# Optimization experiments

Hardware: AMD Instinct MI355X
Metric: run time of the kernel (lower is better)

The kernel has to match this reference:

```python
import jax, jax.numpy as jnp
import numpy as np

N, E, R, L = 50000, 800000, 2, 4
IN, HID, H, D, OUT = 64, 128, 8, 16, 32
EPS = 1e-5


def setup_inputs() -> dict:
    key = jax.random.key(0)
    ks = jax.random.split(key, 12)
    inp = {
        "inputs": jax.random.normal(ks[0], (N, IN), jnp.float32),
        "src": jax.random.randint(ks[1], (R, E), 0, N, jnp.int32),
        "dst": jax.random.randint(ks[2], (R, E), 0, N, jnp.int32),
        "embed_w1": jax.random.normal(ks[3], (IN, HID), jnp.float32) / np.sqrt(IN),
        "embed_gamma": jnp.ones((HID,), jnp.float32),
        "embed_beta": jnp.zeros((HID,), jnp.float32),
        "embed_w2": jax.random.normal(ks[4], (HID, HID), jnp.float32) / np.sqrt(HID),
        "gat_fc": jax.random.normal(ks[5], (L, R, HID, HID), jnp.float32) / np.sqrt(HID),
        "gat_attn_l": jax.random.normal(ks[6], (L, R, H, D), jnp.float32) * 0.1,
        "gat_attn_r": jax.random.normal(ks[7], (L, R, H, D), jnp.float32) * 0.1,
        "gat_bias": jnp.zeros((L, R, HID), jnp.float32),
        "dec_w1": jax.random.normal(ks[8], (HID, HID), jnp.float32) / np.sqrt(HID),
        "dec_gamma": jnp.ones((HID,), jnp.float32),
        "dec_beta": jnp.zeros((HID,), jnp.float32),
        "dec_w2": jax.random.normal(ks[9], (HID, OUT), jnp.float32) / np.sqrt(HID),
    }
    return inp


def _bn(x, gamma, beta):
    # BatchNorm1d in training mode: batch statistics, biased variance
    mean = jnp.mean(x, axis=0)
    var = jnp.mean(jnp.square(x - mean), axis=0)
    return (x - mean) * jax.lax.rsqrt(var + EPS) * gamma + beta


def _gat(h, s, d, W, al, ar, b):
    # DGL GATConv: fc -> per-head attention logits -> edge softmax over dst -> scatter-sum
    feat = (h @ W).reshape(N, H, D)                      # [N,H,D]
    el = jnp.sum(feat * al, axis=-1)                     # [N,H]
    er = jnp.sum(feat * ar, axis=-1)                     # [N,H]
    e = jax.nn.leaky_relu(el[s] + er[d], 0.2)            # [E,H]
    emax = jax.ops.segment_max(e, d, num_segments=N)     # [N,H]
    ex = jnp.exp(e - emax[d])
    denom = jax.ops.segment_sum(ex, d, num_segments=N)   # [N,H]
    alpha = ex / denom[d]                                # [E,H]
    msg = feat[s] * alpha[:, :, None]                    # [E,H,D]
    rst = jax.ops.segment_sum(msg, d, num_segments=N)    # [N,H,D]
    return rst + b.reshape(H, D)


def reference(inputs, src, dst, embed_w1, embed_gamma, embed_beta, embed_w2,
              gat_fc, gat_attn_l, gat_attn_r, gat_bias,
              dec_w1, dec_gamma, dec_beta, dec_w2):
    # MLP2 embed: relu(bn(x@w1)); out = h@w2 + h (residual)
    h = jax.nn.relu(_bn(inputs @ embed_w1, embed_gamma, embed_beta))
    h1 = h @ embed_w2 + h                                # [N,HID]
    for l in range(L):
        acc = jnp.zeros((N, H, D), h1.dtype)
        for r in range(R):  # HeteroGraphConv aggregate='sum'
            acc = acc + _gat(h1, src[r], dst[r], gat_fc[l, r],
                             gat_attn_l[l, r], gat_attn_r[l, r], gat_bias[l, r])
        h2 = jax.nn.leaky_relu(acc, 0.01).reshape(N, HID)
        h1 = h2 + h1                                     # residual
    # decision MLP: relu(bn(h@w1)) @ w2
    hd = jax.nn.relu(_bn(h1 @ dec_w1, dec_gamma, dec_beta))
    return hd @ dec_w2                                   # [N,OUT]
```

## Files before the change

### kernel.cpp

```cpp
#include <hip/hip_runtime.h>
#include <hip/hip_fp16.h>
#include <math.h>

#define NN 50000
#define EE 800000
#define NHEAD 8
#define BN_EPS 1e-5f
#define NBIN 196
#define NBLK 64
#define EPB (EE / NBLK)
#define SCT (2 * NBIN * NBLK)
#define SCHUNK 98

typedef _Float16 half8_t __attribute__((ext_vector_type(8)));
typedef float float4_t __attribute__((ext_vector_type(4)));

__device__ __forceinline__ unsigned fenc(float f) {
  unsigned u = __float_as_uint(f);
  return (u & 0x80000000u) ? ~u : (u | 0x80000000u);
}
__device__ __forceinline__ float fdec(unsigned k) {
  return (k & 0x80000000u) ? __uint_as_float(k & 0x7fffffffu)
                           : __uint_as_float(~k);
}

__device__ __forceinline__ void bn_coef(const float* __restrict__ stats,
                                        const float* __restrict__ gamma,
                                        const float* __restrict__ beta,
                                        int c, float& sc, float& sh) {
  float mean = stats[c] * (1.f / NN);
  float var = fmaxf(stats[128 + c] * (1.f / NN) - mean * mean, 0.f);
  sc = gamma[c] * rsqrtf(var + BN_EPS);
  sh = beta[c] - mean * sc;
}

template <int PAT>
__device__ __forceinline__ float ds_swz(float x) {
  return __int_as_float(__builtin_amdgcn_ds_swizzle(__float_as_int(x), PAT));
}

template <int KDIM, int NC, typename AT, bool ABN, bool RESIDBN, bool STATS,
          bool F16OUT, bool F32OUT>
__global__ __launch_bounds__(256)
void mfma_gemm_k(const AT* __restrict__ A, const _Float16* __restrict__ Bt,
                 const float* __restrict__ bn, const float* __restrict__ gamma,
                 const float* __restrict__ beta, float* __restrict__ statsOut,
                 const _Float16* __restrict__ residh, _Float16* __restrict__ Ch,
                 float* __restrict__ Cf, int M) {
  constexpr int NT = NC / 16;
  const int lane = threadIdx.x & 63, wave = threadIdx.x >> 6;
  const int q = lane >> 4, l16 = lane & 15;
  const int row0 = blockIdx.x * 128 + wave * 32;
  float4_t acc[2][NT];
#pragma unroll
  for (int i = 0; i < 2; ++i)
#pragma unroll
    for (int j = 0; j < NT; ++j) acc[i][j] = (float4_t){0.f, 0.f, 0.f, 0.f};

#pragma unroll
  for (int kk = 0; kk < KDIM / 32; ++kk) {
    float scv[8], shv[8];
    if constexpr (ABN) {
      int kb = kk * 32 + q * 8;
#pragma unroll
      for (int x = 0; x < 8; ++x) bn_coef(bn, gamma, beta, kb + x, scv[x], shv[x]);
    }
    half8_t a[2];
#pragma unroll
    for (int i = 0; i < 2; ++i) {
      int r = row0 + i * 16 + l16;
      r = (r < M) ? r : (M - 1);
      if constexpr (__is_same(AT, _Float16)) {
        half8_t hv = *(const half8_t*)(A + (size_t)r * KDIM + kk * 32 + q * 8);
        if constexpr (ABN) {
#pragma unroll
          for (int x = 0; x < 8; ++x)
            hv[x] = (_Float16)fmaxf((float)hv[x] * scv[x] + shv[x], 0.f);
        }
        a[i] = hv;
      } else {
        const float* ap = (const float*)A + (size_t)r * KDIM + kk * 32 + q * 8;
        float4 v0 = *(const float4*)ap, v1 = *(const float4*)(ap + 4);
        float t[8] = {v0.x, v0.y, v0.z, v0.w, v1.x, v1.y, v1.z, v1.w};
        if constexpr (ABN) {
#pragma unroll
          for (int x = 0; x < 8; ++x) t[x] = fmaxf(t[x] * scv[x] + shv[x], 0.f);
        }
        half8_t hv;
#pragma unroll
        for (int x = 0; x < 8; ++x) hv[x] = (_Float16)t[x];
        a[i] = hv;
      }
    }
#pragma unroll
    for (int j = 0; j < NT; ++j) {
      half8_t b = *(const half8_t*)(Bt + (size_t)(j * 16 + l16) * KDIM + kk * 32 + q * 8);
      acc[0][j] = __builtin_amdgcn_mfma_f32_16x16x32_f16(a[0], b, acc[0][j], 0, 0, 0);
      acc[1][j] = __builtin_amdgcn_mfma_f32_16x16x32_f16(a[1], b, acc[1][j], 0, 0, 0);
    }
  }

  float rsc[NT], rsh[NT];
  if constexpr (RESIDBN) {
#pragma unroll
    for (int j = 0; j < NT; ++j) bn_coef(bn, gamma, beta, j * 16 + l16, rsc[j], rsh[j]);
  }
#pragma unroll
  for (int i = 0; i < 2; ++i)
#pragma unroll
    for (int r = 0; r < 4; ++r) {
      int row = row0 + i * 16 + q * 4 + r;
      if (row >= M) continue;
      float vv[NT];
#pragma unroll
      for (int j = 0; j < NT; ++j) {
        float v = acc[i][j][r];
        if constexpr (RESIDBN) {
          float rv = (float)residh[(size_t)row * NC + j * 16 + l16];
          v += fmaxf(rv * rsc[j] + rsh[j], 0.f);
        }
        vv[j] = v;
        if constexpr (F32OUT) Cf[(size_t)row * NC + j * 16 + l16] = v;
      }
      if constexpr (F16OUT) {
        const bool ev = (l16 & 1) == 0;
#pragma unroll
        for (int jp = 0; jp < NT / 2; ++jp) {
          float a_ = vv[2 * jp], b_ = vv[2 * jp + 1];
          float an = ds_swz<(1 << 10) | 0x1F>(a_);
          float bn_ = ds_swz<(1 << 10) | 0x1F>(b_);
          float lo = ev ? a_ : bn_;
          float hi = ev ? an : b_;
          int jj = ev ? 2 * jp : 2 * jp + 1;
          __half2 hv = __floats2half2_rn(lo, hi);
          ((__half2*)Ch)[((size_t)row * NC + jj * 16 + (l16 & ~1)) >> 1] = hv;
        }
      }
    }

  if constexpr (STATS) {
    static_assert(!STATS || NT == 8, "stats layout assumes NC=128");
    __shared__ float reds[256];
    reds[threadIdx.x] = 0.f;
    __syncthreads();
    float sc_[NT], sq_[NT];
#pragma unroll
    for (int j = 0; j < NT; ++j) {
      float s = 0.f, qq = 0.f;
#pragma unroll
      for (int i = 0; i < 2; ++i)
#pragma unroll
        for (int r = 0; r < 4; ++r) {
          int row = row0 + i * 16 + q * 4 + r;
          float x = (row < M) ? acc[i][j][r] : 0.f;
          s += x; qq += x * x;
        }
      sc_[j] = s; sq_[j] = qq;
    }
#pragma unroll
    for (int j = 0; j < NT; ++j) {
      sc_[j] += __shfl_xor(sc_[j], 16, 64);
      sq_[j] += __shfl_xor(sq_[j], 16, 64);
      sc_[j] += __shfl_xor(sc_[j], 32, 64);
      sq_[j] += __shfl_xor(sq_[j], 32, 64);
    }
    if (lane < 16) {
#pragma unroll
      for (int j = 0; j < NT; ++j) {
        atomicAdd(&reds[j * 16 + l16], sc_[j]);
        atomicAdd(&reds[128 + j * 16 + l16], sq_[j]);
      }
    }
    __syncthreads();
    atomicAdd(&statsOut[threadIdx.x], reds[threadIdx.x]);
  }
}

__global__ __launch_bounds__(256)
void feat_gemm_k(const _Float16* __restrict__ A, const _Float16* __restrict__ Bt,
                 _Float16* __restrict__ feat0, _Float16* __restrict__ feat1,
                 _Float16* __restrict__ el0h, float* __restrict__ er0,
                 _Float16* __restrict__ el1h, float* __restrict__ er1,
                 unsigned* __restrict__ elmax, int M) {
  constexpr int NT = 18;
  const int lane = threadIdx.x & 63, wave = threadIdx.x >> 6;
  const int q = lane >> 4, l16 = lane & 15;
  const int row0 = blockIdx.x * 128 + wave * 32;
  __shared__ unsigned redm[16];
  if (threadIdx.x < 16) redm[threadIdx.x] = 0u;
  float4_t acc[2][NT];
#pragma unroll
  for (int i = 0; i < 2; ++i)
#pragma unroll
    for (int j = 0; j < NT; ++j) acc[i][j] = (float4_t){0.f, 0.f, 0.f, 0.f};

#pragma unroll
  for (int kk = 0; kk < 4; ++kk) {
    half8_t a[2];
#pragma unroll
    for (int i = 0; i < 2; ++i) {
      int r = row0 + i * 16 + l16;
      r = (r < M) ? r : (M - 1);
      a[i] = *(const half8_t*)(A + (size_t)r * 128 + kk * 32 + q * 8);
    }
#pragma unroll
    for (int j = 0; j < NT; ++j) {
      half8_t b = *(const half8_t*)(Bt + (size_t)(j * 16 + l16) * 128 + kk * 32 + q * 8);
      acc[0][j] = __builtin_amdgcn_mfma_f32_16x16x32_f16(a[0], b, acc[0][j], 0, 0, 0);
      acc[1][j] = __builtin_amdgcn_mfma_f32_16x16x32_f16(a[1], b, acc[1][j], 0, 0, 0);
    }
  }

#pragma unroll
  for (int i = 0; i < 2; ++i)
#pragma unroll
    for (int r = 0; r < 4; ++r) {
      int row = row0 + i * 16 + q * 4 + r;
      if (row >= M) continue;
      const bool ev = (l16 & 1) == 0;
#pragma unroll
      for (int jp = 0; jp < 8; ++jp) {
        float a_ = acc[i][2 * jp][r], b_ = acc[i][2 * jp + 1][r];
        float an = ds_swz<(1 << 10) | 0x1F>(a_);
        float bn_ = ds_swz<(1 << 10) | 0x1F>(b_);
        float lo = ev ? a_ : bn_;
        float hi = ev ? an : b_;
        int jj = ev ? 2 * jp : 2 * jp + 1;
        __half2 hv = __floats2half2_rn(lo, hi);
        _Float16* fb = (jj < 8) ? feat0 : feat1;
        int colbase = (jj < 8) ? jj * 16 : (jj - 8) * 16;
        ((__half2*)fb)[((size_t)row * 128 + colbase + (l16 & ~1)) >> 1] = hv;
      }
      {
        float v = acc[i][16][r];
        if (l16 < 8) el0h[(size_t)row * 8 + l16] = (_Float16)v;
        else         er0[(size_t)row * 8 + (l16 - 8)] = v;
        v = acc[i][17][r];
        if (l16 < 8) el1h[(size_t)row * 8 + l16] = (_Float16)v;
        else         er1[(size_t)row * 8 + (l16 - 8)] = v;
      }
    }

  float m0 = -1e30f, m1 = -1e30f;
#pragma unroll
  for (int i = 0; i < 2; ++i)
#pragma unroll
    for (int r = 0; r < 4; ++r) {
      m0 = fmaxf(m0, acc[i][16][r]);
      m1 = fmaxf(m1, acc[i][17][r]);
    }
  m0 = fmaxf(m0, __shfl_xor(m0, 16, 64)); m0 = fmaxf(m0, __shfl_xor(m0, 32, 64));
  m1 = fmaxf(m1, __shfl_xor(m1, 16, 64)); m1 = fmaxf(m1, __shfl_xor(m1, 32, 64));
  __syncthreads();
  if (q == 0 && l16 < 8) {
    atomicMax(&redm[l16], fenc(m0));
    atomicMax(&redm[8 + l16], fenc(m1));
  }
  __syncthreads();
  if (threadIdx.x < 16) atomicMax(&elmax[threadIdx.x], redm[threadIdx.x]);
}

__global__ __launch_bounds__(256)
void build_k(const float* __restrict__ ew1, const float* __restrict__ ew2,
             const float* __restrict__ dw1, const float* __restrict__ dw2,
             const float* __restrict__ gfc, const float* __restrict__ gal,
             const float* __restrict__ gar, _Float16* __restrict__ ew1t,
             _Float16* __restrict__ ew2t, _Float16* __restrict__ dw1t,
             _Float16* __restrict__ dw2t, _Float16* __restrict__ bt,
             float* __restrict__ statsz, unsigned* __restrict__ elmax,
             const int* __restrict__ dstIdx, int* __restrict__ bcnt) {
  const int bid = blockIdx.x;

  if (bid < 172) {
    const float* src; _Float16* dst; int K, N, kt, ct;
    if (bid < 8)       { src = ew1; dst = ew1t; K = 64;  N = 128; int t = bid;      kt = t >> 2; ct = t & 3; }
    else if (bid < 24) { src = ew2; dst = ew2t; K = 128; N = 128; int t = bid - 8;  kt = t >> 2; ct = t & 3; }
    else if (bid < 40) { src = dw1; dst = dw1t; K = 128; N = 128; int t = bid - 24; kt = t >> 2; ct = t & 3; }
    else if (bid < 44) { src = dw2; dst = dw2t; K = 128; N = 32;  int t = bid - 40; kt = t;      ct = 0;     }
    else {
      int idx = bid - 44;
      int mat = idx >> 4, t = idx & 15;
      int b = mat >> 1, r = mat & 1;
      src = gfc + (size_t)(2 * b + r) * 16384;
      dst = bt + (size_t)b * 288 * 128 + (size_t)r * 128 * 128;
      K = 128; N = 128; kt = t >> 2; ct = t & 3;
    }
    __shared__ float tile[32][33];
    int k0 = kt * 32, c0 = ct * 32;
    int tk = threadIdx.x >> 5, tc = threadIdx.x & 31;
#pragma unroll
    for (int it = 0; it < 4; ++it) {
      int k = k0 + tk + it * 8;
      tile[tc][tk + it * 8] = src[(size_t)k * N + c0 + tc];
    }
    __syncthreads();
    int ci = threadIdx.x >> 5, ck = threadIdx.x & 31;
#pragma unroll
    for (int it = 0; it < 4; ++it) {
      int c = c0 + ci + it * 8;
      dst[(size_t)c * K + k0 + ck] = (_Float16)tile[ci + it * 8][ck];
    }
  } else if (bid < 176) {
    int b = bid - 172;
    _Float16* dstL = bt + (size_t)b * 288 * 128;
    for (int idx = threadIdx.x; idx < 32 * 128; idx += 256) {
      int c = 256 + (idx >> 7), k = idx & 127;
      int sub = c - 256, blk = sub >> 3, h = sub & 7;
      int r = blk >> 1;
      const float* attn = (blk & 1) ? gar : gal;
      const float* W = gfc + (size_t)(2 * b + r) * 16384;
      const float* av = attn + (size_t)(2 * b + r) * 128 + h * 16;
      float s = 0.f;
#pragma unroll
      for (int d = 0; d < 16; ++d) s += W[k * 128 + h * 16 + d] * av[d];
      dstL[c * 128 + k] = (_Float16)s;
    }
  } else if (bid == 176) {
    if (threadIdx.x < 64) elmax[threadIdx.x] = 0u;
    for (int i = threadIdx.x; i < 1024; i += 256) statsz[i] = 0.f;
  } else {
    int j = bid - 177;
    int r = j >> 6, blk = j & 63;
    __shared__ int bins[NBIN];
    for (int i = threadIdx.x; i < NBIN; i += 256) bins[i] = 0;
    __syncthreads();
    const int* d = dstIdx + (size_t)r * EE;
    int e0 = blk * EPB;
    for (int e = e0 + threadIdx.x; e < e0 + EPB; e += 256)
      atomicAdd(&bins[d[e] >> 8], 1);
    __syncthreads();
    for (int i = threadIdx.x; i < NBIN; i += 256)
      bcnt[(size_t)(r * NBIN + i) * NBLK + blk] = bins[i];
  }
}

__global__ __launch_bounds__(256)
void scanA_k(int* __restrict__ bcnt, int* __restrict__ totals) {
  __shared__ int sh[256];
  int b = blockIdx.x, t = threadIdx.x;
  int idx = b * 256 + t;
  int v = bcnt[idx];
  sh[t] = v;
  __syncthreads();
#pragma unroll
  for (int off = 1; off < 256; off <<= 1) {
    int tv = (t >= off) ? sh[t - off] : 0;
    __syncthreads();
    sh[t] += tv;
    __syncthreads();
  }
  bcnt[idx] = sh[t] - v;
  if (t == 255) totals[b] = sh[t];
}

__global__ __launch_bounds__(128)
void scanB_k(const int* __restrict__ totals, int* __restrict__ boff) {
  __shared__ int sh[128];
  int t = threadIdx.x;
  int v = (t < SCHUNK) ? totals[t] : 0;
  sh[t] = v;
  __syncthreads();
#pragma unroll
  for (int off = 1; off < 128; off <<= 1) {
    int tv = (t >= off) ? sh[t - off] : 0;
    __syncthreads();
    sh[t] += tv;
    __syncthreads();
  }
  if (t < SCHUNK) boff[t] = sh[t] - v;
}

__global__ __launch_bounds__(256)
void bscat_k(const int* __restrict__ src, const int* __restrict__ dst,
             const int* __restrict__ bcnt, const int* __restrict__ boff,
             unsigned* __restrict__ packed) {
  int r = blockIdx.y, blk = blockIdx.x;
  __shared__ int base[NBIN];
  for (int i = threadIdx.x; i < NBIN; i += 256) {
    int idx = (r * NBIN + i) * NBLK + blk;
    base[i] = bcnt[idx] + boff[idx >> 8];
  }
  __syncthreads();
  const int* d = dst + (size_t)r * EE;
  const int* s = src + (size_t)r * EE;
  int e0 = blk * EPB;
  for (int e = e0 + threadIdx.x; e < e0 + EPB; e += 256) {
    int dd = d[e];
    int pos = atomicAdd(&base[dd >> 8], 1);
    packed[pos] = (unsigned)s[e] | ((unsigned)dd << 16);
  }
}

__global__ __launch_bounds__(256)
void bfin_k(const unsigned* __restrict__ packed, const int* __restrict__ bcnt,
            const int* __restrict__ boff, int* __restrict__ rowptr,
            unsigned short* __restrict__ csr) {
  int f = blockIdx.x;
  int r = f / NBIN, b = f % NBIN;
  __shared__ int deg[256], pref[256], pos[256];
  int start = bcnt[(size_t)f * NBLK] + boff[(f * NBLK) >> 8];
  int end = (f + 1 < 2 * NBIN)
                ? (bcnt[(size_t)(f + 1) * NBLK] + boff[((f + 1) * NBLK) >> 8])
                : 2 * EE;
  deg[threadIdx.x] = 0;
  __syncthreads();
  for (int e = start + threadIdx.x; e < end; e += 256)
    atomicAdd(&deg[(packed[e] >> 16) & 255], 1);
  __syncthreads();
  int v = deg[threadIdx.x];
  pref[threadIdx.x] = v;
  __syncthreads();
#pragma unroll
  for (int off = 1; off < 256; off <<= 1) {
    int tv = (threadIdx.x >= off) ? pref[threadIdx.x - off] : 0;
    __syncthreads();
    pref[threadIdx.x] += tv;
    __syncthreads();
  }
  int excl = pref[threadIdx.x] - v;
  int node = b * 256 + threadIdx.x;
  if (node < NN) rowptr[r * (NN + 1) + node] = start - r * EE + excl;
  if (node == NN) rowptr[r * (NN + 1) + NN] = EE;
  pos[threadIdx.x] = start + excl;
  __syncthreads();
  for (int e = start + threadIdx.x; e < end; e += 256) {
    unsigned pk = packed[e];
    int local = (pk >> 16) & 255;
    int p = atomicAdd(&pos[local], 1);
    csr[p] = (unsigned short)(pk & 0xffffu);
  }
}

__global__ __launch_bounds__(256)
void gat_agg_k(const __half2* __restrict__ f0, const __half2* __restrict__ f1,
               const _Float16* __restrict__ el0h, const float* __restrict__ er0,
               const _Float16* __restrict__ el1h, const float* __restrict__ er1,
               const int* __restrict__ rowptr, const unsigned short* __restrict__ csr,
               const float* __restrict__ b0, const float* __restrict__ b1,
               const unsigned* __restrict__ elmax,
               _Float16* __restrict__ h1h) {
  int n = blockIdx.x * 4 + (threadIdx.x >> 6);
  if (n >= NN) return;
  int lane = threadIdx.x & 63;
  int head = lane >> 3, eslot = lane & 7;
  float er0h = er0[(size_t)n * 8 + head];
  float er1h = er1[(size_t)n * 8 + head];
  float bnd0 = fdec(elmax[head]) + er0h;       bnd0 = fmaxf(bnd0, 0.2f * bnd0);
  float bnd1 = fdec(elmax[8 + head]) + er1h;   bnd1 = fmaxf(bnd1, 0.2f * bnd1);
  int beg0 = rowptr[n], end0 = rowptr[n + 1];
  const int* rp1 = rowptr + (NN + 1);
  int beg1 = rp1[n], end1 = rp1[n + 1];
  const unsigned short* csr1 = csr + EE;
  int len = max(end0 - beg0, end1 - beg1);

  float ls0 = 0.f, a00 = 0.f, a01 = 0.f;
  float ls1 = 0.f, a10 = 0.f, a11 = 0.f;
  for (int t = 0; t < len; t += 8) {
    int t0 = beg0 + t, t1 = beg1 + t;
    int so0 = (int)csr[max(min(t0 + eslot, end0 - 1), 0)];
    int so1 = (int)csr1[max(min(t1 + eslot, end1 - 1), 0)];
    float ev0 = (float)el0h[(size_t)so0 * 8 + head];
    float ev1 = (float)el1h[(size_t)so1 * 8 + head];

    __half2 g0[8], g1[8];
#define LDJ(J)                                                          \
    {                                                                   \
      int sj0 = __builtin_amdgcn_ds_swizzle(so0, ((J) << 5) | 0x18);    \
      int sj1 = __builtin_amdgcn_ds_swizzle(so1, ((J) << 5) | 0x18);    \
      g0[J] = f0[(size_t)sj0 * 64 + lane];                              \
      g1[J] = f1[(size_t)sj1 * 64 + lane];                              \
    }
    LDJ(0) LDJ(1) LDJ(2) LDJ(3) LDJ(4) LDJ(5) LDJ(6) LDJ(7)
#undef LDJ

    float e0 = ev0 + er0h; e0 = fmaxf(e0, 0.2f * e0);
    float p0 = __expf(e0 - bnd0);
    p0 = (t0 + eslot < end0) ? p0 : 0.f;
    float e1 = ev1 + er1h; e1 = fmaxf(e1, 0.2f * e1);
    float p1 = __expf(e1 - bnd1);
    p1 = (t1 + eslot < end1) ? p1 : 0.f;
    ls0 += p0; ls1 += p1;

#define ACCJ(J)                                                     \
    {                                                               \
      float pj0 = ds_swz<((J) << 5) | 0x18>(p0);                    \
      float pj1 = ds_swz<((J) << 5) | 0x18>(p1);                    \
      a00 = fmaf(__low2float(g0[J]), pj0, a00);                     \
      a01 = fmaf(__high2float(g0[J]), pj0, a01);                    \
      a10 = fmaf(__low2float(g1[J]), pj1, a10);                     \
      a11 = fmaf(__high2float(g1[J]), pj1, a11);                    \
    }
    ACCJ(0) ACCJ(1) ACCJ(2) ACCJ(3) ACCJ(4) ACCJ(5) ACCJ(6) ACCJ(7)
#undef ACCJ
  }

  ls0 += ds_swz<(1 << 10) | 0x1F>(ls0);
  ls0 += ds_swz<(2 << 10) | 0x1F>(ls0);
  ls0 += ds_swz<(4 << 10) | 0x1F>(ls0);
  ls1 += ds_swz<(1 << 10) | 0x1F>(ls1);
  ls1 += ds_swz<(2 << 10) | 0x1F>(ls1);
  ls1 += ds_swz<(4 << 10) | 0x1F>(ls1);

  float inv0 = (ls0 > 0.f) ? 1.f / ls0 : 0.f;
  float inv1 = (ls1 > 0.f) ? 1.f / ls1 : 0.f;
  float t0 = a00 * inv0 + a10 * inv1 + b0[lane * 2] + b1[lane * 2];
  float t1 = a01 * inv0 + a11 * inv1 + b0[lane * 2 + 1] + b1[lane * 2 + 1];
  t0 = (t0 > 0.f) ? t0 : 0.01f * t0;
  t1 = (t1 > 0.f) ? t1 : 0.01f * t1;
  __half2* hh = (__half2*)h1h + (size_t)n * 64 + lane;
  float2 h = __half22float2(*hh);
  h.x += t0; h.y += t1;
  *hh = __floats2half2_rn(h.x, h.y);
}

extern "C" void kernel_launch(void* const* d_in, const int* in_sizes, int n_in,
                              void* d_out, int out_size, void* d_ws,
                              size_t ws_size, hipStream_t stream) {
  const float* inputs = (const float*)d_in[0];
  const int* src = (const int*)d_in[1];
  const int* dst = (const int*)d_in[2];
  const float* ew1 = (const float*)d_in[3];
  const float* eg = (const float*)d_in[4];
  const float* eb = (const float*)d_in[5];
  const float* ew2 = (const float*)d_in[6];
  const float* gfc = (const float*)d_in[7];
  const float* gal = (const float*)d_in[8];
  const float* gar = (const float*)d_in[9];
  const float* gb = (const float*)d_in[10];
  const float* dw1 = (const float*)d_in[11];
  const float* dg = (const float*)d_in[12];
  const float* db = (const float*)d_in[13];
  const float* dw2 = (const float*)d_in[14];
  float* out = (float*)d_out;

  char* p = (char*)d_ws;
  _Float16* feat0h = (_Float16*)p;
  _Float16* feat1h = feat0h + (size_t)NN * 128;
  _Float16* ybuf_h = feat0h;
  p += (size_t)NN * 128 * 4;
  _Float16* h1h = (_Float16*)p;     p += (size_t)NN * 128 * 2;
  _Float16* el0h = (_Float16*)p;    p += (size_t)NN * NHEAD * 2;
  float* er0 = (float*)p;           p += (size_t)NN * NHEAD * 4;
  _Float16* el1h = (_Float16*)p;    p += (size_t)NN * NHEAD * 2;
  float* er1 = (float*)p;           p += (size_t)NN * NHEAD * 4;
  float* stats = (float*)p;         p += 1024 * 4;
  float* stats_e = stats;
  float* stats_d = stats + 512;
  _Float16* ew1t = (_Float16*)p;    p += (size_t)64 * 128 * 2;
  _Float16* ew2t = (_Float16*)p;    p += (size_t)128 * 128 * 2;
  _Float16* dw1t = (_Float16*)p;    p += (size_t)128 * 128 * 2;
  _Float16* dw2t = (_Float16*)p;    p += (size_t)32 * 128 * 2;
  _Float16* bt = (_Float16*)p;      p += (size_t)4 * 288 * 128 * 2;
  int* rowptr = (int*)p;            p += (size_t)2 * (NN + 1) * 4;
  unsigned short* csr = (unsigned short*)p;   p += (size_t)2 * EE * 2;
  unsigned* packed = (unsigned*)p;  p += (size_t)2 * EE * 4;
  int* bcnt = (int*)p;              p += (size_t)SCT * 4;
  int* totals = (int*)p;            p += 128 * 4;
  int* boff = (int*)p;              p += 128 * 4;
  unsigned* elmaxAll = (unsigned*)p;

  const int GB = (NN + 127) / 128;

  build_k<<<305, 256, 0, stream>>>(ew1, ew2, dw1, dw2, gfc, gal, gar,
                                   ew1t, ew2t, dw1t, dw2t, bt, stats, elmaxAll,
                                   dst, bcnt);
  scanA_k<<<SCHUNK, 256, 0, stream>>>(bcnt, totals);
  scanB_k<<<1, 128, 0, stream>>>(totals, boff);
  bscat_k<<<dim3(NBLK, 2), 256, 0, stream>>>(src, dst, bcnt, boff, packed);
  bfin_k<<<2 * NBIN, 256, 0, stream>>>(packed, bcnt, boff, rowptr, csr);

  mfma_gemm_k<64, 128, float, false, false, true, true, false>
      <<<GB, 256, 0, stream>>>(inputs, ew1t, nullptr, nullptr, nullptr,
                               stats_e, nullptr, ybuf_h, nullptr, NN);
  mfma_gemm_k<128, 128, _Float16, true, true, false, true, false>
      <<<GB, 256, 0, stream>>>(ybuf_h, ew2t, stats_e, eg, eb, nullptr,
                               ybuf_h, h1h, nullptr, NN);

  for (int l = 0; l < 4; ++l) {
    unsigned* elm = elmaxAll + l * 16;
    feat_gemm_k<<<GB, 256, 0, stream>>>(
        h1h, bt + (size_t)l * 288 * 128, feat0h, feat1h,
        el0h, er0, el1h, er1, elm, NN);
    gat_agg_k<<<(NN + 3) / 4, 256, 0, stream>>>(
        (const __half2*)feat0h, (const __half2*)feat1h, el0h, er0, el1h, er1,
        rowptr, csr, gb + (size_t)(l * 2 + 0) * 128,
        gb + (size_t)(l * 2 + 1) * 128, elm, h1h);
  }

  mfma_gemm_k<128, 128, _Float16, false, false, true, true, false>
      <<<GB, 256, 0, stream>>>(h1h, dw1t, nullptr, nullptr, nullptr, stats_d,
                               nullptr, ybuf_h, nullptr, NN);
  mfma_gemm_k<128, 32, _Float16, true, false, false, false, true>
      <<<GB, 256, 0, stream>>>(ybuf_h, dw2t, stats_d, dg, db, nullptr,
                               nullptr, nullptr, out, NN);
}
```

Measured before the change: 625.7 us.

## Fold chunk-offset scan into consumers and software-pipeline GAT index loads

Removes the single-block scanB kernel launch: each block of bscat_k and bfin_k now recomputes the 98 chunk prefix offsets in shared memory from totals. In gat_agg_k, the CSR source indices are prefetched two iterations ahead and the el attention logits one iteration ahead, so the dependent index->logit->feature gather chain is overlapped across loop iterations. This trades a kernel launch and its serialization for redundant per-block scans, and adds register pressure plus some out-of-range-clamped extra loads in the aggregation loop.

```diff
diff --git a/kernel.cpp b/kernel.cpp
--- a/kernel.cpp
+++ b/kernel.cpp
@@ -353,32 +353,35 @@
   if (t == 255) totals[b] = sh[t];
 }
 
-__global__ __launch_bounds__(128)
-void scanB_k(const int* __restrict__ totals, int* __restrict__ boff) {
-  __shared__ int sh[128];
+__device__ __forceinline__ void chunk_offsets(const int* __restrict__ totals,
+                                              int* __restrict__ boffs) {
+  __shared__ int sh[256];
   int t = threadIdx.x;
   int v = (t < SCHUNK) ? totals[t] : 0;
   sh[t] = v;
   __syncthreads();
 #pragma unroll
-  for (int off = 1; off < 128; off <<= 1) {
+  for (int off = 1; off < 256; off <<= 1) {
     int tv = (t >= off) ? sh[t - off] : 0;
     __syncthreads();
     sh[t] += tv;
     __syncthreads();
   }
-  if (t < SCHUNK) boff[t] = sh[t] - v;
+  if (t < SCHUNK) boffs[t] = sh[t] - v;
+  __syncthreads();
 }
 
 __global__ __launch_bounds__(256)
 void bscat_k(const int* __restrict__ src, const int* __restrict__ dst,
-             const int* __restrict__ bcnt, const int* __restrict__ boff,
+             const int* __restrict__ bcnt, const int* __restrict__ totals,
              unsigned* __restrict__ packed) {
   int r = blockIdx.y, blk = blockIdx.x;
   __shared__ int base[NBIN];
+  __shared__ int boffs[SCHUNK];
+  chunk_offsets(totals, boffs);
   for (int i = threadIdx.x; i < NBIN; i += 256) {
     int idx = (r * NBIN + i) * NBLK + blk;
-    base[i] = bcnt[idx] + boff[idx >> 8];
+    base[i] = bcnt[idx] + boffs[idx >> 8];
   }
   __syncthreads();
   const int* d = dst + (size_t)r * EE;
@@ -393,14 +396,16 @@
 
 __global__ __launch_bounds__(256)
 void bfin_k(const unsigned* __restrict__ packed, const int* __restrict__ bcnt,
-            const int* __restrict__ boff, int* __restrict__ rowptr,
+            const int* __restrict__ totals, int* __restrict__ rowptr,
             unsigned short* __restrict__ csr) {
   int f = blockIdx.x;
   int r = f / NBIN, b = f % NBIN;
+  __shared__ int boffs[SCHUNK];
+  chunk_offsets(totals, boffs);
   __shared__ int deg[256], pref[256], pos[256];
-  int start = bcnt[(size_t)f * NBLK] + boff[(f * NBLK) >> 8];
+  int start = bcnt[(size_t)f * NBLK] + boffs[(f * NBLK) >> 8];
   int end = (f + 1 < 2 * NBIN)
-                ? (bcnt[(size_t)(f + 1) * NBLK] + boff[((f + 1) * NBLK) >> 8])
+                ? (bcnt[(size_t)(f + 1) * NBLK] + boffs[((f + 1) * NBLK) >> 8])
                 : 2 * EE;
   deg[threadIdx.x] = 0;
   __syncthreads();
@@ -453,32 +458,41 @@
   const unsigned short* csr1 = csr + EE;
   int len = max(end0 - beg0, end1 - beg1);
 
+#define CLAMP0(X) max(min((X), end0 - 1), 0)
+#define CLAMP1(X) max(min((X), end1 - 1), 0)
+  int sA0 = (int)csr[CLAMP0(beg0 + eslot)];
+  int sA1 = (int)csr1[CLAMP1(beg1 + eslot)];
+  int sB0 = (int)csr[CLAMP0(beg0 + 8 + eslot)];
+  int sB1 = (int)csr1[CLAMP1(beg1 + 8 + eslot)];
+  float evA0 = (float)el0h[(size_t)sA0 * 8 + head];
+  float evA1 = (float)el1h[(size_t)sA1 * 8 + head];
+
   float ls0 = 0.f, a00 = 0.f, a01 = 0.f;
   float ls1 = 0.f, a10 = 0.f, a11 = 0.f;
   for (int t = 0; t < len; t += 8) {
-    int t0 = beg0 + t, t1 = beg1 + t;
-    int so0 = (int)csr[max(min(t0 + eslot, end0 - 1), 0)];
-    int so1 = (int)csr1[max(min(t1 + eslot, end1 - 1), 0)];
-    float ev0 = (float)el0h[(size_t)so0 * 8 + head];
-    float ev1 = (float)el1h[(size_t)so1 * 8 + head];
+    int sC0 = (int)csr[CLAMP0(beg0 + t + 16 + eslot)];
+    int sC1 = (int)csr1[CLAMP1(beg1 + t + 16 + eslot)];
+    float evB0 = (float)el0h[(size_t)sB0 * 8 + head];
+    float evB1 = (float)el1h[(size_t)sB1 * 8 + head];
 
     __half2 g0[8], g1[8];
 #define LDJ(J)                                                          \
     {                                                                   \
-      int sj0 = __builtin_amdgcn_ds_swizzle(so0, ((J) << 5) | 0x18);    \
-      int sj1 = __builtin_amdgcn_ds_swizzle(so1, ((J) << 5) | 0x18);    \
+      int sj0 = __builtin_amdgcn_ds_swizzle(sA0, ((J) << 5) | 0x18);    \
+      int sj1 = __builtin_amdgcn_ds_swizzle(sA1, ((J) << 5) | 0x18);    \
       g0[J] = f0[(size_t)sj0 * 64 + lane];                              \
       g1[J] = f1[(size_t)sj1 * 64 + lane];                              \
     }
     LDJ(0) LDJ(1) LDJ(2) LDJ(3) LDJ(4) LDJ(5) LDJ(6) LDJ(7)
 #undef LDJ
 
-    float e0 = ev0 + er0h; e0 = fmaxf(e0, 0.2f * e0);
+    int i0 = beg0 + t + eslot, i1 = beg1 + t + eslot;
+    float e0 = evA0 + er0h; e0 = fmaxf(e0, 0.2f * e0);
     float p0 = __expf(e0 - bnd0);
-    p0 = (t0 + eslot < end0) ? p0 : 0.f;
-    float e1 = ev1 + er1h; e1 = fmaxf(e1, 0.2f * e1);
+    p0 = (i0 < end0) ? p0 : 0.f;
+    float e1 = evA1 + er1h; e1 = fmaxf(e1, 0.2f * e1);
     float p1 = __expf(e1 - bnd1);
-    p1 = (t1 + eslot < end1) ? p1 : 0.f;
+    p1 = (i1 < end1) ? p1 : 0.f;
     ls0 += p0; ls1 += p1;
 
 #define ACCJ(J)                                                     \
@@ -492,7 +506,12 @@
     }
     ACCJ(0) ACCJ(1) ACCJ(2) ACCJ(3) ACCJ(4) ACCJ(5) ACCJ(6) ACCJ(7)
 #undef ACCJ
-  }
+
+    sA0 = sB0; sA1 = sB1; sB0 = sC0; sB1 = sC1;
+    evA0 = evB0; evA1 = evB1;
+  }
+#undef CLAMP0
+#undef CLAMP1
 
   ls0 += ds_swz<(1 << 10) | 0x1F>(ls0);
   ls0 += ds_swz<(2 << 10) | 0x1F>(ls0);
@@ -556,7 +575,6 @@
   unsigned* packed = (unsigned*)p;  p += (size_t)2 * EE * 4;
   int* bcnt = (int*)p;              p += (size_t)SCT * 4;
   int* totals = (int*)p;            p += 128 * 4;
-  int* boff = (int*)p;              p += 128 * 4;
   unsigned* elmaxAll = (unsigned*)p;
 
   const int GB = (NN + 127) / 128;
@@ -565,9 +583,8 @@
                                    ew1t, ew2t, dw1t, dw2t, bt, stats, elmaxAll,
                                    dst, bcnt);
   scanA_k<<<SCHUNK, 256, 0, stream>>>(bcnt, totals);
-  scanB_k<<<1, 128, 0, stream>>>(totals, boff);
-  bscat_k<<<dim3(NBLK, 2), 256, 0, stream>>>(src, dst, bcnt, boff, packed);
-  bfin_k<<<2 * NBIN, 256, 0, stream>>>(packed, bcnt, boff, rowptr, csr);
+  bscat_k<<<dim3(NBLK, 2), 256, 0, stream>>>(src, dst, bcnt, totals, packed);
+  bfin_k<<<2 * NBIN, 256, 0, stream>>>(packed, bcnt, totals, rowptr, csr);
 
   mfma_gemm_k<64, 128, float, false, false, true, true, false>
       <<<GB, 256, 0, stream>>>(inputs, ew1t, nullptr, nullptr, nullptr,
```

Measured after the change: 631.4 us. No clear change (+0.9%).

## Fold embed GEMM into setup kernel and inline chunk-offset scan

Applied to the files above, without the earlier changes.

The first embedding GEMM (inputs @ ew1 with BatchNorm statistics) now runs as extra blocks of the setup kernel, which builds ew1 in fp16 directly in shared memory. The separate scanB kernel is removed, and each bscat/bfin block recomputes the chunk offsets from the totals itself. Stats zeroing moves to a memset. Together these cut two kernel launches and let the embed GEMM overlap the histogram work, at the cost of redundant per-block scans and a larger, more register- and LDS-heavy setup kernel.

```diff
diff --git a/kernel.cpp b/kernel.cpp
--- a/kernel.cpp
+++ b/kernel.cpp
@@ -260,6 +260,108 @@
   if (threadIdx.x < 16) atomicMax(&elmax[threadIdx.x], redm[threadIdx.x]);
 }
 
+__device__ __forceinline__ void embed1_block(
+    const float* __restrict__ A, const float* __restrict__ ew1,
+    float* __restrict__ statsOut, _Float16* __restrict__ Ch, int gb, int M) {
+  constexpr int NT = 8, BS = 72;
+  __shared__ _Float16 blds[128 * BS];
+  __shared__ float reds[256];
+  for (int L = threadIdx.x; L < 128 * 64; L += 256) {
+    int c = L >> 6, k = L & 63;
+    blds[c * BS + k] = (_Float16)ew1[k * 128 + c];
+  }
+  reds[threadIdx.x] = 0.f;
+  __syncthreads();
+
+  const int lane = threadIdx.x & 63, wave = threadIdx.x >> 6;
+  const int q = lane >> 4, l16 = lane & 15;
+  const int row0 = gb * 128 + wave * 32;
+  float4_t acc[2][NT];
+#pragma unroll
+  for (int i = 0; i < 2; ++i)
+#pragma unroll
+    for (int j = 0; j < NT; ++j) acc[i][j] = (float4_t){0.f, 0.f, 0.f, 0.f};
+
+#pragma unroll
+  for (int kk = 0; kk < 2; ++kk) {
+    half8_t a[2];
+#pragma unroll
+    for (int i = 0; i < 2; ++i) {
+      int r = row0 + i * 16 + l16;
+      r = (r < M) ? r : (M - 1);
+      const float* ap = A + (size_t)r * 64 + kk * 32 + q * 8;
+      float4 v0 = *(const float4*)ap, v1 = *(const float4*)(ap + 4);
+      float t[8] = {v0.x, v0.y, v0.z, v0.w, v1.x, v1.y, v1.z, v1.w};
+      half8_t hv;
+#pragma unroll
+      for (int x = 0; x < 8; ++x) hv[x] = (_Float16)t[x];
+      a[i] = hv;
+    }
+#pragma unroll
+    for (int j = 0; j < NT; ++j) {
+      half8_t b = *(const half8_t*)(blds + (size_t)(j * 16 + l16) * BS + kk * 32 + q * 8);
+      acc[0][j] = __builtin_amdgcn_mfma_f32_16x16x32_f16(a[0], b, acc[0][j], 0, 0, 0);
+      acc[1][j] = __builtin_amdgcn_mfma_f32_16x16x32_f16(a[1], b, acc[1][j], 0, 0, 0);
+    }
+  }
+
+#pragma unroll
+  for (int i = 0; i < 2; ++i)
+#pragma unroll
+    for (int r = 0; r < 4; ++r) {
+      int row = row0 + i * 16 + q * 4 + r;
+      if (row >= M) continue;
+      float vv[NT];
+#pragma unroll
+      for (int j = 0; j < NT; ++j) vv[j] = acc[i][j][r];
+      const bool ev = (l16 & 1) == 0;
+#pragma unroll
+      for (int jp = 0; jp < NT / 2; ++jp) {
+        float a_ = vv[2 * jp], b_ = vv[2 * jp + 1];
+        float an = ds_swz<(1 << 10) | 0x1F>(a_);
+        float bn_ = ds_swz<(1 << 10) | 0x1F>(b_);
+        float lo = ev ? a_ : bn_;
+        float hi = ev ? an : b_;
+        int jj = ev ? 2 * jp : 2 * jp + 1;
+        __half2 hv = __floats2half2_rn(lo, hi);
+        ((__half2*)Ch)[((size_t)row * 128 + jj * 16 + (l16 & ~1)) >> 1] = hv;
+      }
+    }
+
+  {
+    float sc_[NT], sq_[NT];
+#pragma unroll
+    for (int j = 0; j < NT; ++j) {
+      float s = 0.f, qq = 0.f;
+#pragma unroll
+      for (int i = 0; i < 2; ++i)
+#pragma unroll
+        for (int r = 0; r < 4; ++r) {
+          int row = row0 + i * 16 + q * 4 + r;
+          float x = (row < M) ? acc[i][j][r] : 0.f;
+          s += x; qq += x * x;
+        }
+      sc_[j] = s; sq_[j] = qq;
+    }
+#pragma unroll
+    for (int j = 0; j < NT; ++j) {
+      sc_[j] += __shfl_xor(sc_[j], 16, 64);
+      sq_[j] += __shfl_xor(sq_[j], 16, 64);
+      sc_[j] += __shfl_xor(sc_[j], 32, 64);
+      sq_[j] += __shfl_xor(sq_[j], 32, 64);
+    }
+    if (lane < 16) {
+#pragma unroll
+      for (int j = 0; j < NT; ++j) {
+        atomicAdd(&reds[j * 16 + l16], sc_[j]);
+        atomicAdd(&reds[128 + j * 16 + l16], sq_[j]);
+      }
+    }
+    __syncthreads();
+    atomicAdd(&statsOut[threadIdx.x], reds[threadIdx.x]);
+  }
+}
+
 __global__ __launch_bounds__(256)
 void build_k(const float* __restrict__ ew1, const float* __restrict__ ew2,
              const float* __restrict__ dw1, const float* __restrict__ dw2,
@@ -267,8 +369,10 @@
              const float* __restrict__ gar, _Float16* __restrict__ ew1t,
              _Float16* __restrict__ ew2t, _Float16* __restrict__ dw1t,
              _Float16* __restrict__ dw2t, _Float16* __restrict__ bt,
-             float* __restrict__ statsz, unsigned* __restrict__ elmax,
-             const int* __restrict__ dstIdx, int* __restrict__ bcnt) {
+             unsigned* __restrict__ elmax,
+             const int* __restrict__ dstIdx, int* __restrict__ bcnt,
+             const float* __restrict__ inputs, float* __restrict__ stats_e,
+             _Float16* __restrict__ ybuf_h) {
   const int bid = blockIdx.x;
 
   if (bid < 172) {
@@ -317,8 +421,7 @@
     }
   } else if (bid == 176) {
     if (threadIdx.x < 64) elmax[threadIdx.x] = 0u;
-    for (int i = threadIdx.x; i < 1024; i += 256) statsz[i] = 0.f;
-  } else {
+  } else if (bid < 305) {
     int j = bid - 177;
     int r = j >> 6, blk = j & 63;
     __shared__ int bins[NBIN];
@@ -331,6 +434,8 @@
     __syncthreads();
     for (int i = threadIdx.x; i < NBIN; i += 256)
       bcnt[(size_t)(r * NBIN + i) * NBLK + blk] = bins[i];
+  } else {
+    embed1_block(inputs, ew1, stats_e, ybuf_h, bid - 305, NN);
   }
 }
 
@@ -353,32 +458,35 @@
   if (t == 255) totals[b] = sh[t];
 }
 
-__global__ __launch_bounds__(128)
-void scanB_k(const int* __restrict__ totals, int* __restrict__ boff) {
-  __shared__ int sh[128];
+__device__ __forceinline__ void chunk_offsets(const int* __restrict__ totals,
+                                              int* __restrict__ boffs) {
+  __shared__ int sh[256];
   int t = threadIdx.x;
   int v = (t < SCHUNK) ? totals[t] : 0;
   sh[t] = v;
   __syncthreads();
 #pragma unroll
-  for (int off = 1; off < 128; off <<= 1) {
+  for (int off = 1; off < 256; off <<= 1) {
     int tv = (t >= off) ? sh[t - off] : 0;
     __syncthreads();
     sh[t] += tv;
     __syncthreads();
   }
-  if (t < SCHUNK) boff[t] = sh[t] - v;
+  if (t < SCHUNK) boffs[t] = sh[t] - v;
+  __syncthreads();
 }
 
 __global__ __launch_bounds__(256)
 void bscat_k(const int* __restrict__ src, const int* __restrict__ dst,
-             const int* __restrict__ bcnt, const int* __restrict__ boff,
+             const int* __restrict__ bcnt, const int* __restrict__ totals,
              unsigned* __restrict__ packed) {
   int r = blockIdx.y, blk = blockIdx.x;
   __shared__ int base[NBIN];
+  __shared__ int boffs[SCHUNK];
+  chunk_offsets(totals, boffs);
   for (int i = threadIdx.x; i < NBIN; i += 256) {
     int idx = (r * NBIN + i) * NBLK + blk;
-    base[i] = bcnt[idx] + boff[idx >> 8];
+    base[i] = bcnt[idx] + boffs[idx >> 8];
   }
   __syncthreads();
   const int* d = dst + (size_t)r * EE;
@@ -393,14 +501,16 @@
 
 __global__ __launch_bounds__(256)
 void bfin_k(const unsigned* __restrict__ packed, const int* __restrict__ bcnt,
-            const int* __restrict__ boff, int* __restrict__ rowptr,
+            const int* __restrict__ totals, int* __restrict__ rowptr,
             unsigned short* __restrict__ csr) {
   int f = blockIdx.x;
   int r = f / NBIN, b = f % NBIN;
+  __shared__ int boffs[SCHUNK];
+  chunk_offsets(totals, boffs);
   __shared__ int deg[256], pref[256], pos[256];
-  int start = bcnt[(size_t)f * NBLK] + boff[(f * NBLK) >> 8];
+  int start = bcnt[(size_t)f * NBLK] + boffs[(f * NBLK) >> 8];
   int end = (f + 1 < 2 * NBIN)
-                ? (bcnt[(size_t)(f + 1) * NBLK] + boff[((f + 1) * NBLK) >> 8])
+                ? (bcnt[(size_t)(f + 1) * NBLK] + boffs[((f + 1) * NBLK) >> 8])
                 : 2 * EE;
   deg[threadIdx.x] = 0;
   __syncthreads();
@@ -556,22 +666,19 @@
   unsigned* packed = (unsigned*)p;  p += (size_t)2 * EE * 4;
   int* bcnt = (int*)p;              p += (size_t)SCT * 4;
   int* totals = (int*)p;            p += 128 * 4;
-  int* boff = (int*)p;              p += 128 * 4;
   unsigned* elmaxAll = (unsigned*)p;
 
   const int GB = (NN + 127) / 128;
 
-  build_k<<<305, 256, 0, stream>>>(ew1, ew2, dw1, dw2, gfc, gal, gar,
-                                   ew1t, ew2t, dw1t, dw2t, bt, stats, elmaxAll,
-                                   dst, bcnt);
+  hipMemsetAsync(stats, 0, 1024 * 4, stream);
+
+  build_k<<<696, 256, 0, stream>>>(ew1, ew2, dw1, dw2, gfc, gal, gar,
+                                   ew1t, ew2t, dw1t, dw2t, bt, elmaxAll,
+                                   dst, bcnt, inputs, stats_e, ybuf_h);
   scanA_k<<<SCHUNK, 256, 0, stream>>>(bcnt, totals);
-  scanB_k<<<1, 128, 0, stream>>>(totals, boff);
-  bscat_k<<<dim3(NBLK, 2), 256, 0, stream>>>(src, dst, bcnt, boff, packed);
-  bfin_k<<<2 * NBIN, 256, 0, stream>>>(packed, bcnt, boff, rowptr, csr);
-
-  mfma_gemm_k<64, 128, float, false, false, true, true, false>
-      <<<GB, 256, 0, stream>>>(inputs, ew1t, nullptr, nullptr, nullptr,
-                               stats_e, nullptr, ybuf_h, nullptr, NN);
+  bscat_k<<<dim3(NBLK, 2), 256, 0, stream>>>(src, dst, bcnt, totals, packed);
+  bfin_k<<<2 * NBIN, 256, 0, stream>>>(packed, bcnt, totals, rowptr, csr);
+
   mfma_gemm_k<128, 128, _Float16, true, true, false, true, false>
       <<<GB, 256, 0, stream>>>(ybuf_h, ew2t, stats_e, eg, eb, nullptr,
                                ybuf_h, h1h, nullptr, NN);
```

Measured after the change: 619.8 us. About the same (-0.9%).
